# Kernel optimization log

Hardware: AMD Instinct MI355X
Metric: run time of the kernel (lower is better)

Reference implementation:

```python
import jax, jax.numpy as jnp
import numpy as np

N = 50000       # num_nodes
E = 800000      # num_edges (avg degree 16)
DIN = 128       # input_dim
DOUT = 128      # output_dim
H = 4           # num_heads
HD = DOUT // H  # head_dim = 32


def setup_inputs() -> dict:
    key = jax.random.key(0)
    ks = jax.random.split(key, 9)
    x = jax.random.normal(ks[0], (N, DIN), dtype=jnp.float32)
    edge_index = jax.random.randint(ks[1], (2, E), 0, N, dtype=jnp.int64)
    s = 1.0 / np.sqrt(DIN)
    Wq = jax.random.uniform(ks[2], (DOUT, DIN), jnp.float32, -s, s)
    bq = jax.random.uniform(ks[3], (DOUT,), jnp.float32, -s, s)
    Wk = jax.random.uniform(ks[4], (DOUT, DIN), jnp.float32, -s, s)
    bk = jax.random.uniform(ks[5], (DOUT,), jnp.float32, -s, s)
    Wv = jax.random.uniform(ks[6], (DOUT, DIN), jnp.float32, -s, s)
    bv = jax.random.uniform(ks[7], (DOUT,), jnp.float32, -s, s)
    att = jax.random.normal(ks[8], (H, 2 * HD), dtype=jnp.float32)  # nn.Parameter(randn)
    return {"x": x, "edge_index": edge_index, "Wq": Wq, "bq": bq,
            "Wk": Wk, "bk": bk, "Wv": Wv, "bv": bv, "att": att}


def reference(x, edge_index, Wq, bq, Wk, bk, Wv, bv, att):
    n = x.shape[0]
    q = (x @ Wq.T + bq).reshape(n, H, HD)
    k = (x @ Wk.T + bk).reshape(n, H, HD)
    v = (x @ Wv.T + bv).reshape(n, H, HD)
    row, col = edge_index[0], edge_index[1]

    # scores = leaky_relu(sum(cat([q[row],k[col]]) * att)) computed without concat
    a_q, a_k = att[:, :HD], att[:, HD:]                       # [H,HD] each
    scores = jnp.einsum('ehd,hd->eh', q[row], a_q) \
           + jnp.einsum('ehd,hd->eh', k[col], a_k)            # [E,H]
    scores = jax.nn.leaky_relu(scores, 0.2)

    # segment-softmax over edges grouped by destination node (col), per head
    m = jax.ops.segment_max(scores, col, num_segments=n)      # [N,H]
    m = jnp.where(jnp.isfinite(m), m, 0.0)                    # empty segments -> -inf guard
    e = jnp.exp(scores - m[col])                              # [E,H]
    denom = jax.ops.segment_sum(e, col, num_segments=n)       # [N,H]
    w_edge = e / denom[col]                                   # softmax per dst segment

    # attention_weights[i] = mean over incoming edges of softmax weights; 0 if deg==0
    deg = jax.ops.segment_sum(jnp.ones((col.shape[0],), jnp.float32), col,
                              num_segments=n)                 # [N]
    w_sum = jax.ops.segment_sum(w_edge, col, num_segments=n)  # [N,H]
    attn_w = jnp.where(deg[:, None] > 0, w_sum / jnp.maximum(deg, 1.0)[:, None], 0.0)

    # output[dst] += attn_w[dst] * v[src], summed over edges
    msgs = attn_w[col][:, :, None] * v[row]                   # [E,H,HD]
    out = jax.ops.segment_sum(msgs, col, num_segments=n)      # [N,H,HD]
    return out.reshape(n, DOUT)                               # dropout: eval mode (identity)
```

## Files before the change

kernel.cpp:

```cpp
#include <hip/hip_runtime.h>


#define N_NODES 50000
#define N_EDGES 800000
#define SPAN    96
#define NBUCK   521
#define CAP     2304
#define EPB     2048
#define NCHUNK  391
#define GEMMB   391

#define OFF_SORTED 12800000
#define OFF_CURSOR 17601536

typedef __attribute__((ext_vector_type(8))) short short8;
typedef __attribute__((ext_vector_type(4))) float f32x4;

__device__ __forceinline__ unsigned int pack_bf16_rne(float a, float b) {
    unsigned int ua = __float_as_uint(a), ub = __float_as_uint(b);
    unsigned int ha = (ua + 0x7FFFu + ((ua >> 16) & 1u)) >> 16;
    unsigned int hb = (ub + 0x7FFFu + ((ub >> 16) & 1u)) >> 16;
    return ha | (hb << 16);
}
__device__ __forceinline__ unsigned short bf16_rne(float a) {
    unsigned int ua = __float_as_uint(a);
    return (unsigned short)((ua + 0x7FFFu + ((ua >> 16) & 1u)) >> 16);
}
__device__ __forceinline__ float bflo(unsigned int u) { return __uint_as_float(u << 16); }
__device__ __forceinline__ float bfhi(unsigned int u) { return __uint_as_float(u & 0xFFFF0000u); }

__global__ __launch_bounds__(512) void fused_gemm_scatter(
        const float* __restrict__ x, const float* __restrict__ Wv,
        const float* __restrict__ bv, unsigned int* __restrict__ vh,
        const int* __restrict__ ei, int* __restrict__ Cursor,
        unsigned int* __restrict__ sorted) {
    __shared__ __align__(16) unsigned char smem[128 * 68 * 4];
    __shared__ int s_wide;
    int t = threadIdx.x;

    if (blockIdx.x < GEMMB) {
        unsigned int* wB = (unsigned int*)smem;
        for (int q = t; q < 8192; q += 512) {
            int o = q >> 6, k2 = q & 63;
            float2 wp = ((const float2*)Wv)[q];
            wB[o * 68 + k2] = pack_bf16_rne(wp.x, wp.y);
        }
        __syncthreads();

        int lane = t & 63, w = t >> 6;
        int quad = lane >> 4, lc = lane & 15;
        int n0 = blockIdx.x * 128 + w * 16;

        int arow = n0 + lc;
        int arowc = min(arow, N_NODES - 1);
        const float4* xrow = (const float4*)(x + (size_t)arowc * 128);

        f32x4 acc[8];
        #pragma unroll
        for (int ot = 0; ot < 8; ++ot) acc[ot] = (f32x4){0.f, 0.f, 0.f, 0.f};

        #pragma unroll
        for (int ks = 0; ks < 4; ++ks) {
            float4 f0 = xrow[ks * 8 + quad * 2];
            float4 f1 = xrow[ks * 8 + quad * 2 + 1];
            uint4 a4;
            a4.x = pack_bf16_rne(f0.x, f0.y);
            a4.y = pack_bf16_rne(f0.z, f0.w);
            a4.z = pack_bf16_rne(f1.x, f1.y);
            a4.w = pack_bf16_rne(f1.z, f1.w);
            short8 af = *(const short8*)&a4;
            #pragma unroll
            for (int ot = 0; ot < 8; ++ot) {
                uint4 b4 = *(const uint4*)&wB[(ot * 16 + lc) * 68 + ks * 16 + quad * 4];
                short8 bf = *(const short8*)&b4;
                acc[ot] = __builtin_amdgcn_mfma_f32_16x16x32_bf16(af, bf, acc[ot], 0, 0, 0);
            }
        }

        #pragma unroll
        for (int ot = 0; ot < 8; ++ot) {
            int o = ot * 16 + lc;
            float bb = bv[o];
            #pragma unroll
            for (int r = 0; r < 4; ++r) {
                int node = n0 + quad * 4 + r;
                unsigned short u = bf16_rne(acc[ot][r] + bb);
                unsigned int partner = (unsigned int)__shfl_xor((int)u, 1, 64);
                if ((lane & 1) == 0 && node < N_NODES) {
                    unsigned int pair = (unsigned int)u | (partner << 16);
                    vh[(size_t)node * 64 + (o >> 1)] = pair;
                }
            }
        }
    } else {
        unsigned int* w = (unsigned int*)smem;
        int* h    = (int*)(smem + EPB * 4);
        int* base = (int*)(smem + EPB * 4 + NBUCK * 4);
        for (int j = t; j < NBUCK; j += 512) h[j] = 0;
        if (t < 64) {
            int nz = (ei[2 * t + 1] != 0) ? 1 : 0;
            unsigned long long b = __ballot(nz);
            if (t == 0) s_wide = (b == 0ULL) ? 1 : 0;
        }
        __syncthreads();
        int wide = s_wide;
        int e0 = (blockIdx.x - GEMMB) * EPB;

        #pragma unroll
        for (int k = 0; k < EPB / 512; ++k) {
            int e = e0 + k * 512 + t;
            if (e < N_EDGES) {
                int r, c;
                if (wide) {
                    r = (int)((const uint2*)ei)[e].x;
                    c = (int)((const uint2*)ei)[N_EDGES + e].x;
                } else {
                    r = ei[e];
                    c = ei[N_EDGES + e];
                }
                w[k * 512 + t] = ((unsigned int)c << 16) | (unsigned int)r;
                atomicAdd(&h[c / SPAN], 1);
            } else {
                w[k * 512 + t] = 0xFFFFFFFFu;
            }
        }
        __syncthreads();
        for (int j = t; j < NBUCK; j += 512) {
            int cnt = h[j];
            base[j] = cnt ? atomicAdd(&Cursor[j], cnt) : 0;
            h[j] = 0;
        }
        __syncthreads();
        #pragma unroll
        for (int k = 0; k < EPB / 512; ++k) {
            unsigned int ww = w[k * 512 + t];
            if (ww != 0xFFFFFFFFu) {
                int bin = (int)(ww >> 16) / SPAN;
                int p = base[bin] + atomicAdd(&h[bin], 1);
                if (p < CAP)
                    sorted[(size_t)bin * CAP + p] = ww;
            }
        }
    }
}

__global__ __launch_bounds__(512) void gather_kernel(const unsigned int* __restrict__ vh,
                                                     const unsigned int* __restrict__ sorted,
                                                     const int* __restrict__ Cursor,
                                                     float* __restrict__ out) {
    __shared__ unsigned int ww[CAP];
    __shared__ unsigned short rl[CAP];
    __shared__ int deg[SPAN];
    __shared__ int startc[SPAN];
    __shared__ int curp[SPAN];
    __shared__ int sc_s[128];
    int t = threadIdx.x;
    int b = blockIdx.x;
    int nb0 = b * SPAN;
    int span = min(SPAN, N_NODES - nb0);
    int cnt = min(Cursor[b], CAP);
    if (t < SPAN) deg[t] = 0;
    __syncthreads();

    const unsigned int* run = sorted + (size_t)b * CAP;
    for (int i = t; i < cnt; i += 512) {
        unsigned int v = run[i];
        ww[i] = v;
        atomicAdd(&deg[(int)(v >> 16) - nb0], 1);
    }
    __syncthreads();

    if (t < 128) sc_s[t] = (t < SPAN) ? deg[t] : 0;
    __syncthreads();
    for (int off = 1; off < 128; off <<= 1) {
        int y = (t < 128 && t >= off) ? sc_s[t - off] : 0;
        __syncthreads();
        if (t < 128) sc_s[t] += y;
        __syncthreads();
    }
    if (t < SPAN) { startc[t] = sc_s[t] - deg[t]; curp[t] = 0; }
    __syncthreads();

    for (int i = t; i < cnt; i += 512) {
        unsigned int v = ww[i];
        int ln = (int)(v >> 16) - nb0;
        int p = startc[ln] + atomicAdd(&curp[ln], 1);
        rl[p] = (unsigned short)(v & 0xFFFFu);
    }
    __syncthreads();

    int lane = t & 63, wid = t >> 6;
    int half = lane >> 5;
    int li = lane & 31;
    const uint2* v2 = (const uint2*)vh;

    for (int ln = wid; ln < span; ln += 8) {
        int s0 = startc[ln], d = deg[ln];
        double c0a = 0., c1a = 0., c2a = 0., c3a = 0.;
        double c0b = 0., c1b = 0., c2b = 0., c3b = 0.;
        int j = 0;
        for (; j + 8 <= d; j += 8) {
            int rA0 = rl[s0 + j + 0], rB0 = rl[s0 + j + 1];
            int rA1 = rl[s0 + j + 2], rB1 = rl[s0 + j + 3];
            int rA2 = rl[s0 + j + 4], rB2 = rl[s0 + j + 5];
            int rA3 = rl[s0 + j + 6], rB3 = rl[s0 + j + 7];
            uint2 p0 = v2[(size_t)(half ? rB0 : rA0) * 32 + li];
            uint2 p1 = v2[(size_t)(half ? rB1 : rA1) * 32 + li];
            uint2 p2 = v2[(size_t)(half ? rB2 : rA2) * 32 + li];
            uint2 p3 = v2[(size_t)(half ? rB3 : rA3) * 32 + li];
            c0a += (double)bflo(p0.x); c1a += (double)bfhi(p0.x);
            c2a += (double)bflo(p0.y); c3a += (double)bfhi(p0.y);
            c0b += (double)bflo(p1.x); c1b += (double)bfhi(p1.x);
            c2b += (double)bflo(p1.y); c3b += (double)bfhi(p1.y);
            c0a += (double)bflo(p2.x); c1a += (double)bfhi(p2.x);
            c2a += (double)bflo(p2.y); c3a += (double)bfhi(p2.y);
            c0b += (double)bflo(p3.x); c1b += (double)bfhi(p3.x);
            c2b += (double)bflo(p3.y); c3b += (double)bfhi(p3.y);
        }
        for (; j + 2 <= d; j += 2) {
            int rA = rl[s0 + j], rB = rl[s0 + j + 1];
            uint2 p0 = v2[(size_t)(half ? rB : rA) * 32 + li];
            c0a += (double)bflo(p0.x); c1a += (double)bfhi(p0.x);
            c2a += (double)bflo(p0.y); c3a += (double)bfhi(p0.y);
        }
        if (j < d) {
            int rA = rl[s0 + j];
            uint2 p0 = v2[(size_t)rA * 32 + li];
            if (!half) {
                c0a += (double)bflo(p0.x); c1a += (double)bfhi(p0.x);
                c2a += (double)bflo(p0.y); c3a += (double)bfhi(p0.y);
            }
        }
        double c0 = c0a + c0b, c1 = c1a + c1b, c2 = c2a + c2b, c3 = c3a + c3b;
        c0 += __shfl_xor(c0, 32, 64);
        c1 += __shfl_xor(c1, 32, 64);
        c2 += __shfl_xor(c2, 32, 64);
        c3 += __shfl_xor(c3, 32, 64);
        if (half == 0) {
            double sc = (d > 0) ? 1.0 / (double)d : 0.0;
            float4 res = {(float)(c0 * sc), (float)(c1 * sc),
                          (float)(c2 * sc), (float)(c3 * sc)};
            ((float4*)out)[(size_t)(nb0 + ln) * 32 + li] = res;
        }
    }
}

extern "C" void kernel_launch(void* const* d_in, const int* in_sizes, int n_in,
                              void* d_out, int out_size, void* d_ws, size_t ws_size,
                              hipStream_t stream) {
    const float* x  = (const float*)d_in[0];
    const int*   ei = (const int*)d_in[1];
    const float* Wv = (const float*)d_in[6];
    const float* bv = (const float*)d_in[7];
    float* out = (float*)d_out;

    char* ws = (char*)d_ws;
    unsigned int* vh     = (unsigned int*)(ws);
    unsigned int* sorted = (unsigned int*)(ws + OFF_SORTED);
    int*          Cursor = (int*)(ws + OFF_CURSOR);

    hipMemsetAsync(Cursor, 0, NBUCK * sizeof(int), stream);
    fused_gemm_scatter<<<GEMMB + NCHUNK, 512, 0, stream>>>(x, Wv, bv, vh,
                                                           ei, Cursor, sorted);
    gather_kernel<<<NBUCK, 512, 0, stream>>>(vh, sorted, Cursor, out);
}
```

Before: 146.5 us.

## Gather four edges per wave with 16-byte loads and shrink node span

The gather loop now splits each 64-lane wave into four 16-lane groups. Each group reads a full 256-byte bf16 row with uint4 loads, so one wave handles four edges at a time instead of two, and the partial sums are combined with two xor-shuffle steps. The node span per bucket drops from 96 to 64, which raises the bucket count and block count, and the capacity and workspace offsets are adjusted to match. This aims to issue fewer, wider memory requests and expose more parallelism, at the cost of extra shuffle reductions, more double-precision accumulators, and more edge-tail waste on low-degree nodes.

```diff
diff --git a/kernel.cpp b/kernel.cpp
--- a/kernel.cpp
+++ b/kernel.cpp
@@ -3,15 +3,15 @@
 
 #define N_NODES 50000
 #define N_EDGES 800000
-#define SPAN    96
-#define NBUCK   521
-#define CAP     2304
+#define SPAN    64
+#define NBUCK   782
+#define CAP     1536
 #define EPB     2048
 #define NCHUNK  391
 #define GEMMB   391
 
 #define OFF_SORTED 12800000
-#define OFF_CURSOR 17601536
+#define OFF_CURSOR 17604608
 
 typedef __attribute__((ext_vector_type(8))) short short8;
 typedef __attribute__((ext_vector_type(4))) float f32x4;
@@ -153,7 +153,7 @@
     __shared__ int deg[SPAN];
     __shared__ int startc[SPAN];
     __shared__ int curp[SPAN];
-    __shared__ int sc_s[128];
+    __shared__ int sc_s[SPAN];
     int t = threadIdx.x;
     int b = blockIdx.x;
     int nb0 = b * SPAN;
@@ -170,12 +170,12 @@
     }
     __syncthreads();
 
-    if (t < 128) sc_s[t] = (t < SPAN) ? deg[t] : 0;
-    __syncthreads();
-    for (int off = 1; off < 128; off <<= 1) {
-        int y = (t < 128 && t >= off) ? sc_s[t - off] : 0;
-        __syncthreads();
-        if (t < 128) sc_s[t] += y;
+    if (t < SPAN) sc_s[t] = deg[t];
+    __syncthreads();
+    for (int off = 1; off < SPAN; off <<= 1) {
+        int y = (t < SPAN && t >= off) ? sc_s[t - off] : 0;
+        __syncthreads();
+        if (t < SPAN) sc_s[t] += y;
         __syncthreads();
     }
     if (t < SPAN) { startc[t] = sc_s[t] - deg[t]; curp[t] = 0; }
@@ -190,57 +190,75 @@
     __syncthreads();
 
     int lane = t & 63, wid = t >> 6;
-    int half = lane >> 5;
-    int li = lane & 31;
-    const uint2* v2 = (const uint2*)vh;
+    int qg = lane >> 4;
+    int li = lane & 15;
+    const uint4* v4 = (const uint4*)vh;
 
     for (int ln = wid; ln < span; ln += 8) {
         int s0 = startc[ln], d = deg[ln];
-        double c0a = 0., c1a = 0., c2a = 0., c3a = 0.;
-        double c0b = 0., c1b = 0., c2b = 0., c3b = 0.;
+        double c0 = 0., c1 = 0., c2 = 0., c3 = 0.;
+        double c4 = 0., c5 = 0., c6 = 0., c7 = 0.;
         int j = 0;
-        for (; j + 8 <= d; j += 8) {
-            int rA0 = rl[s0 + j + 0], rB0 = rl[s0 + j + 1];
-            int rA1 = rl[s0 + j + 2], rB1 = rl[s0 + j + 3];
-            int rA2 = rl[s0 + j + 4], rB2 = rl[s0 + j + 5];
-            int rA3 = rl[s0 + j + 6], rB3 = rl[s0 + j + 7];
-            uint2 p0 = v2[(size_t)(half ? rB0 : rA0) * 32 + li];
-            uint2 p1 = v2[(size_t)(half ? rB1 : rA1) * 32 + li];
-            uint2 p2 = v2[(size_t)(half ? rB2 : rA2) * 32 + li];
-            uint2 p3 = v2[(size_t)(half ? rB3 : rA3) * 32 + li];
-            c0a += (double)bflo(p0.x); c1a += (double)bfhi(p0.x);
-            c2a += (double)bflo(p0.y); c3a += (double)bfhi(p0.y);
-            c0b += (double)bflo(p1.x); c1b += (double)bfhi(p1.x);
-            c2b += (double)bflo(p1.y); c3b += (double)bfhi(p1.y);
-            c0a += (double)bflo(p2.x); c1a += (double)bfhi(p2.x);
-            c2a += (double)bflo(p2.y); c3a += (double)bfhi(p2.y);
-            c0b += (double)bflo(p3.x); c1b += (double)bfhi(p3.x);
-            c2b += (double)bflo(p3.y); c3b += (double)bfhi(p3.y);
-        }
-        for (; j + 2 <= d; j += 2) {
-            int rA = rl[s0 + j], rB = rl[s0 + j + 1];
-            uint2 p0 = v2[(size_t)(half ? rB : rA) * 32 + li];
-            c0a += (double)bflo(p0.x); c1a += (double)bfhi(p0.x);
-            c2a += (double)bflo(p0.y); c3a += (double)bfhi(p0.y);
+        for (; j + 16 <= d; j += 16) {
+            int r0 = rl[s0 + j + qg];
+            int r1 = rl[s0 + j + 4 + qg];
+            int r2 = rl[s0 + j + 8 + qg];
+            int r3 = rl[s0 + j + 12 + qg];
+            uint4 p0 = v4[(size_t)r0 * 16 + li];
+            uint4 p1 = v4[(size_t)r1 * 16 + li];
+            uint4 p2 = v4[(size_t)r2 * 16 + li];
+            uint4 p3 = v4[(size_t)r3 * 16 + li];
+            c0 += (double)bflo(p0.x); c1 += (double)bfhi(p0.x);
+            c2 += (double)bflo(p0.y); c3 += (double)bfhi(p0.y);
+            c4 += (double)bflo(p0.z); c5 += (double)bfhi(p0.z);
+            c6 += (double)bflo(p0.w); c7 += (double)bfhi(p0.w);
+            c0 += (double)bflo(p1.x); c1 += (double)bfhi(p1.x);
+            c2 += (double)bflo(p1.y); c3 += (double)bfhi(p1.y);
+            c4 += (double)bflo(p1.z); c5 += (double)bfhi(p1.z);
+            c6 += (double)bflo(p1.w); c7 += (double)bfhi(p1.w);
+            c0 += (double)bflo(p2.x); c1 += (double)bfhi(p2.x);
+            c2 += (double)bflo(p2.y); c3 += (double)bfhi(p2.y);
+            c4 += (double)bflo(p2.z); c5 += (double)bfhi(p2.z);
+            c6 += (double)bflo(p2.w); c7 += (double)bfhi(p2.w);
+            c0 += (double)bflo(p3.x); c1 += (double)bfhi(p3.x);
+            c2 += (double)bflo(p3.y); c3 += (double)bfhi(p3.y);
+            c4 += (double)bflo(p3.z); c5 += (double)bfhi(p3.z);
+            c6 += (double)bflo(p3.w); c7 += (double)bfhi(p3.w);
+        }
+        for (; j + 4 <= d; j += 4) {
+            int r0 = rl[s0 + j + qg];
+            uint4 p0 = v4[(size_t)r0 * 16 + li];
+            c0 += (double)bflo(p0.x); c1 += (double)bfhi(p0.x);
+            c2 += (double)bflo(p0.y); c3 += (double)bfhi(p0.y);
+            c4 += (double)bflo(p0.z); c5 += (double)bfhi(p0.z);
+            c6 += (double)bflo(p0.w); c7 += (double)bfhi(p0.w);
         }
         if (j < d) {
-            int rA = rl[s0 + j];
-            uint2 p0 = v2[(size_t)rA * 32 + li];
-            if (!half) {
-                c0a += (double)bflo(p0.x); c1a += (double)bfhi(p0.x);
-                c2a += (double)bflo(p0.y); c3a += (double)bfhi(p0.y);
-            }
-        }
-        double c0 = c0a + c0b, c1 = c1a + c1b, c2 = c2a + c2b, c3 = c3a + c3b;
-        c0 += __shfl_xor(c0, 32, 64);
-        c1 += __shfl_xor(c1, 32, 64);
-        c2 += __shfl_xor(c2, 32, 64);
-        c3 += __shfl_xor(c3, 32, 64);
-        if (half == 0) {
+            int idx = j + qg;
+            if (idx < d) {
+                uint4 p0 = v4[(size_t)rl[s0 + idx] * 16 + li];
+                c0 += (double)bflo(p0.x); c1 += (double)bfhi(p0.x);
+                c2 += (double)bflo(p0.y); c3 += (double)bfhi(p0.y);
+                c4 += (double)bflo(p0.z); c5 += (double)bfhi(p0.z);
+                c6 += (double)bflo(p0.w); c7 += (double)bfhi(p0.w);
+            }
+        }
+        c0 += __shfl_xor(c0, 16, 64); c0 += __shfl_xor(c0, 32, 64);
+        c1 += __shfl_xor(c1, 16, 64); c1 += __shfl_xor(c1, 32, 64);
+        c2 += __shfl_xor(c2, 16, 64); c2 += __shfl_xor(c2, 32, 64);
+        c3 += __shfl_xor(c3, 16, 64); c3 += __shfl_xor(c3, 32, 64);
+        c4 += __shfl_xor(c4, 16, 64); c4 += __shfl_xor(c4, 32, 64);
+        c5 += __shfl_xor(c5, 16, 64); c5 += __shfl_xor(c5, 32, 64);
+        c6 += __shfl_xor(c6, 16, 64); c6 += __shfl_xor(c6, 32, 64);
+        c7 += __shfl_xor(c7, 16, 64); c7 += __shfl_xor(c7, 32, 64);
+        if (qg < 2) {
             double sc = (d > 0) ? 1.0 / (double)d : 0.0;
-            float4 res = {(float)(c0 * sc), (float)(c1 * sc),
-                          (float)(c2 * sc), (float)(c3 * sc)};
-            ((float4*)out)[(size_t)(nb0 + ln) * 32 + li] = res;
+            float4 res;
+            if (qg == 0) res = (float4){(float)(c0 * sc), (float)(c1 * sc),
+                                        (float)(c2 * sc), (float)(c3 * sc)};
+            else         res = (float4){(float)(c4 * sc), (float)(c5 * sc),
+                                        (float)(c6 * sc), (float)(c7 * sc)};
+            *(float4*)(out + (size_t)(nb0 + ln) * 128 + li * 8 + qg * 4) = res;
         }
     }
 }
```

New measurement: 151.2 us. 1.03x slower.
